# Kernel optimization log

Measured on AMD Instinct MI355X. Metric: run time of the kernel, lower is better.

Reference implementation:

```python
import jax, jax.numpy as jnp
import numpy as np

H = 8          # num_head
HD = 64        # head_dim = hidden_dim // num_head
WIN = 33       # atten_window_size (odd)
MIN_SCORE = -1e9


def setup_inputs() -> dict:
    key = jax.random.key(0)
    ks = jax.random.split(key, 12)
    B, S, D = 8, 4096, 512
    scale = 1.0 / np.sqrt(D).astype(np.float32)

    def lin_w(k):
        return jax.random.normal(k, (D, D), jnp.float32) * scale

    return {
        "query": jax.random.normal(ks[0], (B, S, D), jnp.float32),
        "key": jax.random.normal(ks[1], (B, S, D), jnp.float32),
        "value": jax.random.normal(ks[2], (B, S, D), jnp.float32),
        "mask": jax.random.randint(ks[3], (B, S), 0, 2).astype(bool),
        "Wq": lin_w(ks[4]), "bq": jax.random.normal(ks[5], (D,), jnp.float32) * 0.02,
        "Wk": lin_w(ks[6]), "bk": jax.random.normal(ks[7], (D,), jnp.float32) * 0.02,
        "Wv": lin_w(ks[8]), "bv": jax.random.normal(ks[9], (D,), jnp.float32) * 0.02,
        "Wo": lin_w(ks[10]), "bo": jax.random.normal(ks[11], (D,), jnp.float32) * 0.02,
    }


def reference(query, key, value, mask, Wq, bq, Wk, bk, Wv, bv, Wo, bo):
    B, S, D = query.shape
    half = min(WIN // 2, S // 2)

    def proj_split(x, W, b):
        # nn.Linear: x @ W.T + b; then split heads and flatten (B,H) -> B*H
        y = x @ W.T + b
        return y.reshape(B, S, H, HD).transpose(0, 2, 1, 3).reshape(B * H, S, HD)

    q = proj_split(query, Wq, bq)   # [BH, S, HD]
    k = proj_split(key, Wk, bk)
    v = proj_split(value, Wv, bv)
    # mask expanded over heads; True = masked (LocalAttention semantics)
    m = jnp.broadcast_to(mask[:, None, :], (B, H, S)).reshape(B * H, S)

    # banded scores: one [BH, S] vector per window offset (no sqrt(head_dim) scaling,
    # faithful to LocalAttention)
    scores = []
    for off in range(-half, half + 1):
        if off < 0:
            w = jnp.sum(q[:, -off:] * k[:, :off], axis=-1)
            w = jnp.where(m[:, :off], MIN_SCORE, w)
            w = jnp.pad(w, ((0, 0), (-off, 0)), constant_values=MIN_SCORE)
        elif off == 0:
            w = jnp.where(m, MIN_SCORE, jnp.sum(q * k, axis=-1))
        else:
            w = jnp.sum(q[:, :-off] * k[:, off:], axis=-1)
            w = jnp.where(m[:, off:], MIN_SCORE, w)
            w = jnp.pad(w, ((0, 0), (0, off)), constant_values=MIN_SCORE)
        scores.append(w)
    probs = jax.nn.softmax(jnp.stack(scores, axis=-1), axis=-1)  # [BH, S, 2*half+1]

    # weighted gather of values along the band (dropout=0 -> identity)
    out = jnp.zeros_like(v)
    for i, off in enumerate(range(-half, half + 1)):
        p = probs[:, :, i:i + 1]
        if off < 0:
            out = out + jnp.pad(p[:, -off:] * v[:, :off], ((0, 0), (-off, 0), (0, 0)))
        elif off == 0:
            out = out + p * v
        else:
            out = out + jnp.pad(p[:, :-off] * v[:, off:], ((0, 0), (0, off), (0, 0)))

    out = out.reshape(B, H, S, HD).transpose(0, 2, 1, 3).reshape(B, S, D)
    return out @ Wo.T + bo
```

## Files before the change

### kernel.cpp

```cpp
#include <hip/hip_runtime.h>
#include <hip/hip_bf16.h>
#include <stdint.h>

#define BB 8
#define SS 4096
#define DD 512
#define HH 8
#define HDIM 64

typedef unsigned short u16;
typedef __attribute__((ext_vector_type(4))) float f32x4;
typedef __attribute__((ext_vector_type(4))) short s16x4;
typedef __attribute__((ext_vector_type(8))) short s16x8;

__device__ __forceinline__ u16 f2bf(float f) {
  uint32_t x = __builtin_bit_cast(uint32_t, f);
  x += 0x7fffu + ((x >> 16) & 1u);
  return (u16)(x >> 16);
}
__device__ __forceinline__ float bf2f(u16 u) {
  uint32_t x = (uint32_t)u << 16;
  return __builtin_bit_cast(float, x);
}

__device__ __forceinline__ void gld_lds16(const u16* g, u16* l) {
  __builtin_amdgcn_global_load_lds((const __attribute__((address_space(1))) void*)g,
                                   (__attribute__((address_space(3))) void*)l, 16, 0, 0);
}

__global__ void cvt_f32_bf16(const float* __restrict__ in, u16* __restrict__ out, int n8) {
  int i = blockIdx.x * blockDim.x + threadIdx.x;
  const int stride = gridDim.x * blockDim.x;
  for (; i < n8; i += stride) {
    const f32x4 a0 = *(const f32x4*)(in + (size_t)i * 8);
    const f32x4 a1 = *(const f32x4*)(in + (size_t)i * 8 + 4);
    s16x8 pk;
#pragma unroll
    for (int j = 0; j < 4; ++j) pk[j] = (short)f2bf(a0[j]);
#pragma unroll
    for (int j = 0; j < 4; ++j) pk[4 + j] = (short)f2bf(a1[j]);
    *(s16x8*)(out + (size_t)i * 8) = pk;
  }
}

__global__ void cvt_weights(const float* __restrict__ w0, const float* __restrict__ w1,
                            const float* __restrict__ w2, const float* __restrict__ w3,
                            u16* __restrict__ out) {
  int i = blockIdx.x * blockDim.x + threadIdx.x;
  const int n = DD * DD;
  if (i < n) {
    out[i]         = f2bf(w0[i]);
    out[n + i]     = f2bf(w1[i]);
    out[2 * n + i] = f2bf(w2[i]);
    out[3 * n + i] = f2bf(w3[i]);
  }
}

__global__ void mask_unpack(const void* __restrict__ mraw, uint8_t* __restrict__ mk, int n) {
  __shared__ int bad[3];
  __shared__ int mode;
  const int t = threadIdx.x;
  if (t < 3) bad[t] = 0;
  __syncthreads();
  const uint32_t* w = (const uint32_t*)mraw;
  const uint32_t x = w[t];
  const bool w01 = (x == 0u) || (x == 1u);
  const uint32_t ob = x | (x >> 8) | (x >> 16) | (x >> 24);
  const bool u01 = ((ob & 0xFEu) == 0u);
  if (!w01) atomicAdd(&bad[0], 1);
  if (!u01) atomicAdd(&bad[1], 1);
  __syncthreads();
  if (t == 0) mode = (bad[0] == 0) ? 0 : (bad[1] == 0 ? 1 : 2);
  __syncthreads();
  const int md = mode;
  for (int i = blockIdx.x * 256 + t; i < n; i += gridDim.x * 256) {
    uint8_t v;
    if (md == 0)      v = (uint8_t)(w[i] & 1u);
    else if (md == 1) v = ((const uint8_t*)mraw)[i] ? 1 : 0;
    else              v = (w[i] != 0u) ? 1 : 0;
    mk[i] = v;
  }
}

template <typename TC>
__global__ __launch_bounds__(256, 2)
void gemm97(const u16* __restrict__ A, const u16* __restrict__ Bw,
            const float* __restrict__ bias, TC* __restrict__ C,
            int M, int N, int K) {
  __shared__ u16 sA[128 * 32];
  __shared__ u16 sB[128 * 32];

  const int tid = threadIdx.x;
  const int lane = tid & 63, wv = tid >> 6;
  const int wr = (wv >> 1) * 64, wc = (wv & 1) * 64;
  const int c = lane & 15, g = lane >> 4;
  const int lid = blockIdx.x;
  const int rb = (lid >> 5) * 8 + (lid & 7);
  const int cb = (lid >> 3) & 3;
  const int col0 = cb * 128, row0 = rb * 128;

  const int srow = tid >> 2, scol = (tid & 3) * 8;
  const u16* a_src = A + (size_t)(row0 + srow) * K + scol;
  const u16* b_src = Bw + (size_t)(col0 + srow) * K + scol;
  u16* sa0 = &sA[wv * 512];
  u16* sa1 = &sA[2048 + wv * 512];
  u16* sb0 = &sB[wv * 512];
  u16* sb1 = &sB[2048 + wv * 512];

  f32x4 acc[4][4];
#pragma unroll
  for (int a = 0; a < 4; ++a)
#pragma unroll
    for (int b = 0; b < 4; ++b) acc[a][b] = (f32x4){0.f, 0.f, 0.f, 0.f};

  const int nkt = K / 32;
  for (int kt = 0; kt < nkt; ++kt) {
    __syncthreads();
    const int ko = kt * 32;
    gld_lds16(a_src + ko, sa0);
    gld_lds16(a_src + (size_t)64 * K + ko, sa1);
    gld_lds16(b_src + ko, sb0);
    gld_lds16(b_src + (size_t)64 * K + ko, sb1);
    __syncthreads();

    s16x8 af[4], bq[4];
#pragma unroll
    for (int mf = 0; mf < 4; ++mf) af[mf] = *(const s16x8*)&sA[(wr + mf * 16 + c) * 32 + g * 8];
#pragma unroll
    for (int nf = 0; nf < 4; ++nf) bq[nf] = *(const s16x8*)&sB[(wc + nf * 16 + c) * 32 + g * 8];
#pragma unroll
    for (int mf = 0; mf < 4; ++mf)
#pragma unroll
      for (int nf = 0; nf < 4; ++nf)
        acc[mf][nf] = __builtin_amdgcn_mfma_f32_16x16x32_bf16(af[mf], bq[nf], acc[mf][nf], 0, 0, 0);
  }

#pragma unroll
  for (int nf = 0; nf < 4; ++nf) {
    const int col = col0 + wc + nf * 16 + c;
    const float bv = bias[col];
#pragma unroll
    for (int mf = 0; mf < 4; ++mf) {
#pragma unroll
      for (int i = 0; i < 4; ++i) {
        const int row = row0 + wr + mf * 16 + g * 4 + i;
        const float v = acc[mf][nf][i] + bv;
        if constexpr (sizeof(TC) == 4) C[(size_t)row * N + col] = v;
        else                           C[(size_t)row * N + col] = (TC)f2bf(v);
      }
    }
  }
}

__device__ __forceinline__ void hilo8(const f32x4& a0, const f32x4& a1, s16x8& h, s16x8& l) {
#pragma unroll
  for (int j = 0; j < 4; ++j) {
    const float f = a0[j];
    const u16 hb = f2bf(f);
    h[j] = (short)hb;
    l[j] = (short)f2bf(f - bf2f(hb));
  }
#pragma unroll
  for (int j = 0; j < 4; ++j) {
    const float f = a1[j];
    const u16 hb = f2bf(f);
    h[4 + j] = (short)hb;
    l[4 + j] = (short)f2bf(f - bf2f(hb));
  }
}

__global__ __launch_bounds__(256, 4)
void attn_mfma(const float* __restrict__ Qp, const float* __restrict__ Kp,
               const float* __restrict__ Vp, const uint8_t* __restrict__ mk,
               u16* __restrict__ O) {
  __shared__ u16 sKh[96 * 72];
  __shared__ u16 sKl[96 * 68];
  __shared__ u16 sVT[64 * 104];
  __shared__ float sM[96];

  const int bh = blockIdx.x;
  const int b = bh >> 3, h = bh & 7;
  const int s0 = blockIdx.y * 64;
  const int tid = threadIdx.x;

#pragma unroll
  for (int it = 0; it < 3; ++it) {
    const int item = tid + it * 256;
    const int row = item >> 3, j = item & 7;
    const int ks = j >> 2, g2 = j & 3;
    const int gr = s0 - 16 + row;
    f32x4 a0 = (f32x4){0.f, 0.f, 0.f, 0.f}, a1 = (f32x4){0.f, 0.f, 0.f, 0.f};
    if (gr >= 0 && gr < SS) {
      const float* kp = Kp + ((size_t)(b * SS + gr)) * DD + h * HDIM + ks * 32 + g2 * 4;
      a0 = *(const f32x4*)kp;
      a1 = *(const f32x4*)(kp + 16);
    }
    s16x8 hh, ll;
    hilo8(a0, a1, hh, ll);
    *(s16x8*)&sKh[row * 72 + j * 8] = hh;
    *(s16x4*)&sKl[row * 68 + j * 8]     = (s16x4){ll[0], ll[1], ll[2], ll[3]};
    *(s16x4*)&sKl[row * 68 + j * 8 + 4] = (s16x4){ll[4], ll[5], ll[6], ll[7]};
  }
#pragma unroll
  for (int it = 0; it < 6; ++it) {
    const int item = tid + it * 256;
    const int k = item >> 4, dg = item & 15;
    const int gr = s0 - 16 + k;
    f32x4 vv = (f32x4){0.f, 0.f, 0.f, 0.f};
    if (gr >= 0 && gr < SS)
      vv = *(const f32x4*)(Vp + ((size_t)(b * SS + gr)) * DD + h * HDIM + dg * 4);
    const int ks = k >> 5, rem = k & 31, hf = rem >> 4, q = rem & 15;
    const int g2 = q >> 2, i2 = q & 3;
    const int pos = (ks * 4 + g2) * 8 + hf * 4 + i2;
#pragma unroll
    for (int i = 0; i < 4; ++i) sVT[(dg * 4 + i) * 104 + pos] = f2bf(vv[i]);
  }
  for (int r = tid; r < 96; r += 256) {
    const int gr = s0 - 16 + r;
    sM[r] = (gr < 0 || gr >= SS || mk[b * SS + gr]) ? 1.f : 0.f;
  }
  __syncthreads();

  const int wv = tid >> 6, lane = tid & 63;
  const int c = lane & 15, g = lane >> 4;
  const int qloc = wv * 16 + c;
  const int qrow = s0 + qloc;

  const float* qp = Qp + ((size_t)(b * SS + qrow)) * DD + h * HDIM;
  s16x8 qh[2], qlo[2];
#pragma unroll
  for (int ks = 0; ks < 2; ++ks) {
    const f32x4 a0 = *(const f32x4*)(qp + 32 * ks + 4 * g);
    const f32x4 a1 = *(const f32x4*)(qp + 32 * ks + 16 + 4 * g);
    hilo8(a0, a1, qh[ks], qlo[ks]);
  }

  f32x4 st[6];
#pragma unroll
  for (int kt = 0; kt < 6; ++kt) st[kt] = (f32x4){0.f, 0.f, 0.f, 0.f};
#pragma unroll
  for (int kt = 0; kt < 6; ++kt) {
    const int rb72 = (kt * 16 + c) * 72;
    const int rb68 = (kt * 16 + c) * 68;
#pragma unroll
    for (int ks = 0; ks < 2; ++ks) {
      const s16x8 kh = *(const s16x8*)&sKh[rb72 + ks * 32 + g * 8];
      const s16x4 l0 = *(const s16x4*)&sKl[rb68 + ks * 32 + g * 8];
      const s16x4 l1 = *(const s16x4*)&sKl[rb68 + ks * 32 + g * 8 + 4];
      const s16x8 kl = (s16x8){l0[0], l0[1], l0[2], l0[3], l1[0], l1[1], l1[2], l1[3]};
      st[kt] = __builtin_amdgcn_mfma_f32_16x16x32_bf16(kh, qh[ks], st[kt], 0, 0, 0);
      st[kt] = __builtin_amdgcn_mfma_f32_16x16x32_bf16(kh, qlo[ks], st[kt], 0, 0, 0);
      st[kt] = __builtin_amdgcn_mfma_f32_16x16x32_bf16(kl, qh[ks], st[kt], 0, 0, 0);
    }
  }

  float mx = -3.0e9f;
#pragma unroll
  for (int kt = 0; kt < 6; ++kt) {
#pragma unroll
    for (int i = 0; i < 4; ++i) {
      const int kl_ = kt * 16 + 4 * g + i;
      const int delta = kl_ - 16 - qloc;
      float v;
      if (delta < -16 || delta > 16) v = -2.0e9f;
      else if (sM[kl_] != 0.f)       v = -1.0e9f;
      else                           v = st[kt][i];
      st[kt][i] = v;
      mx = fmaxf(mx, v);
    }
  }
  mx = fmaxf(mx, __shfl_xor(mx, 16));
  mx = fmaxf(mx, __shfl_xor(mx, 32));
  float sum = 0.f;
#pragma unroll
  for (int kt = 0; kt < 6; ++kt) {
#pragma unroll
    for (int i = 0; i < 4; ++i) {
      const float e = __expf(st[kt][i] - mx);
      st[kt][i] = e;
      sum += e;
    }
  }
  sum += __shfl_xor(sum, 16);
  sum += __shfl_xor(sum, 32);
  const float inv = 1.f / sum;

  s16x8 ph[3];
#pragma unroll
  for (int ks = 0; ks < 3; ++ks) {
#pragma unroll
    for (int i = 0; i < 4; ++i) {
      ph[ks][i]     = (short)f2bf(st[2 * ks][i]);
      ph[ks][4 + i] = (short)f2bf(st[2 * ks + 1][i]);
    }
  }

  f32x4 ot[4];
#pragma unroll
  for (int dt = 0; dt < 4; ++dt) ot[dt] = (f32x4){0.f, 0.f, 0.f, 0.f};
#pragma unroll
  for (int dt = 0; dt < 4; ++dt) {
    const int rbv = (dt * 16 + c) * 104;
#pragma unroll
    for (int ks = 0; ks < 3; ++ks) {
      const s16x8 vh = *(const s16x8*)&sVT[rbv + ks * 32 + g * 8];
      ot[dt] = __builtin_amdgcn_mfma_f32_16x16x32_bf16(vh, ph[ks], ot[dt], 0, 0, 0);
    }
  }

  u16* op = O + ((size_t)(b * SS + qrow)) * DD + h * HDIM;
#pragma unroll
  for (int dt = 0; dt < 4; ++dt) {
    s16x4 pk;
#pragma unroll
    for (int i = 0; i < 4; ++i) pk[i] = (short)f2bf(ot[dt][i] * inv);
    *(s16x4*)&op[dt * 16 + 4 * g] = pk;
  }
}

__global__ __launch_bounds__(256)
void attn_win(const u16* __restrict__ Qp, const u16* __restrict__ Kp,
              const u16* __restrict__ Vp, const uint8_t* __restrict__ mk,
              u16* __restrict__ O) {
  constexpr int KR = 96;
  __shared__ float sK[KR][HDIM];
  __shared__ float sV[KR][HDIM];
  __shared__ float sM[KR];

  const int bh = blockIdx.x;
  const int b = bh >> 3, h = bh & 7;
  const int s0 = blockIdx.y * 64;
  const int tid = threadIdx.x;

  for (int c = tid; c < KR * 16; c += 256) {
    const int row = c >> 4, c4 = c & 15;
    const int gr = s0 - 16 + row;
    float kv[4], vv[4];
    if (gr >= 0 && gr < SS) {
      const size_t base = ((size_t)(b * SS + gr)) * DD + h * HDIM + c4 * 4;
      const s16x4 kk = *(const s16x4*)(Kp + base);
      const s16x4 vx = *(const s16x4*)(Vp + base);
#pragma unroll
      for (int i = 0; i < 4; ++i) { kv[i] = bf2f((u16)kk[i]); vv[i] = bf2f((u16)vx[i]); }
    } else {
#pragma unroll
      for (int i = 0; i < 4; ++i) { kv[i] = 0.f; vv[i] = 0.f; }
    }
#pragma unroll
    for (int i = 0; i < 4; ++i) {
      const int d = c4 * 4 + i;
      const int pd = (d & 15) * 4 + (d >> 4);
      sK[row][pd] = kv[i];
      sV[row][pd] = vv[i];
    }
  }
  for (int r = tid; r < KR; r += 256) {
    const int gr = s0 - 16 + r;
    sM[r] = (gr < 0 || gr >= SS || mk[b * SS + gr]) ? 1.f : 0.f;
  }
  __syncthreads();

  const int wv = tid >> 6, lane = tid & 63;
  const int g = lane >> 4, d16 = lane & 15;

  for (int rr = 0; rr < 16; rr += 4) {
    const int lr = wv * 16 + rr + g;
    const int srow = s0 + lr;
    const u16* qp = Qp + ((size_t)(b * SS + srow)) * DD + h * HDIM;
    float q0 = bf2f(qp[d16]), q1 = bf2f(qp[d16 + 16]), q2 = bf2f(qp[d16 + 32]), q3 = bf2f(qp[d16 + 48]);
    float sc[33];
#pragma unroll
    for (int o = 0; o < 33; ++o) {
      const f32x4 kk = *(const f32x4*)&sK[lr + o][d16 * 4];
      float p = q0 * kk[0] + q1 * kk[1] + q2 * kk[2] + q3 * kk[3];
      p += __shfl_xor(p, 1);
      p += __shfl_xor(p, 2);
      p += __shfl_xor(p, 4);
      p += __shfl_xor(p, 8);
      sc[o] = (sM[lr + o] != 0.f) ? -1.0e9f : p;
    }
    float mx = sc[0];
#pragma unroll
    for (int o = 1; o < 33; ++o) mx = fmaxf(mx, sc[o]);
    float sum = 0.f;
#pragma unroll
    for (int o = 0; o < 33; ++o) { const float e = __expf(sc[o] - mx); sc[o] = e; sum += e; }
    const float inv = 1.f / sum;
    f32x4 acc = (f32x4){0.f, 0.f, 0.f, 0.f};
#pragma unroll
    for (int o = 0; o < 33; ++o) {
      const f32x4 vx = *(const f32x4*)&sV[lr + o][d16 * 4];
      acc += (sc[o] * inv) * vx;
    }
    u16* op = O + ((size_t)(b * SS + srow)) * DD + h * HDIM;
    op[d16]      = f2bf(acc[0]);
    op[d16 + 16] = f2bf(acc[1]);
    op[d16 + 32] = f2bf(acc[2]);
    op[d16 + 48] = f2bf(acc[3]);
  }
}

extern "C" void kernel_launch(void* const* d_in, const int* in_sizes, int n_in,
                              void* d_out, int out_size, void* d_ws, size_t ws_size,
                              hipStream_t stream) {
  const float* query = (const float*)d_in[0];
  const float* key   = (const float*)d_in[1];
  const float* value = (const float*)d_in[2];
  const void*  mraw  = d_in[3];
  const float* Wq = (const float*)d_in[4];
  const float* bq = (const float*)d_in[5];
  const float* Wk = (const float*)d_in[6];
  const float* bk = (const float*)d_in[7];
  const float* Wv = (const float*)d_in[8];
  const float* bv = (const float*)d_in[9];
  const float* Wo = (const float*)d_in[10];
  const float* bo = (const float*)d_in[11];

  const int M = BB * SS, N = DD, K = DD;

  char* ws = (char*)d_ws;
  size_t off = 0;
  auto carve = [&](size_t bytes) -> char* {
    char* p = ws + off;
    off = (off + bytes + 255) & ~(size_t)255;
    return p;
  };
  u16* wAll   = (u16*)carve((size_t)4 * DD * DD * sizeof(u16));
  uint8_t* mk = (uint8_t*)carve((size_t)BB * SS);
  u16* Xb     = (u16*)carve((size_t)M * DD * 2);

  const size_t qkv_f32 = (size_t)M * DD * 4;
  const bool f32p = (off + 3 * qkv_f32 + 1024) <= ws_size;

  cvt_weights<<<(DD * DD + 255) / 256, 256, 0, stream>>>(Wq, Wk, Wv, Wo, wAll);
  mask_unpack<<<16, 256, 0, stream>>>(mraw, mk, BB * SS);

  const int n8 = M * DD / 8;
  const dim3 gc(2048);
  const dim3 gg((M / 128) * (N / 128));
  const dim3 ga(BB * HH, SS / 64);
  u16* AO = Xb;

  if (f32p) {
    float* Qf = (float*)carve(qkv_f32);
    float* Kf = (float*)carve(qkv_f32);
    float* Vf = (float*)carve(qkv_f32);
    cvt_f32_bf16<<<gc, 256, 0, stream>>>(query, Xb, n8);
    gemm97<float><<<gg, 256, 0, stream>>>(Xb, wAll,               bq, Qf, M, N, K);
    cvt_f32_bf16<<<gc, 256, 0, stream>>>(key, Xb, n8);
    gemm97<float><<<gg, 256, 0, stream>>>(Xb, wAll + DD * DD,     bk, Kf, M, N, K);
    cvt_f32_bf16<<<gc, 256, 0, stream>>>(value, Xb, n8);
    gemm97<float><<<gg, 256, 0, stream>>>(Xb, wAll + 2 * DD * DD, bv, Vf, M, N, K);
    attn_mfma<<<ga, 256, 0, stream>>>(Qf, Kf, Vf, mk, AO);
  } else {
    const size_t qkv_b16 = (size_t)M * DD * 2;
    u16* Qb = (u16*)carve(qkv_b16);
    u16* Kb = (u16*)carve(qkv_b16);
    u16* Vb = (u16*)carve(qkv_b16);
    cvt_f32_bf16<<<gc, 256, 0, stream>>>(query, Xb, n8);
    gemm97<u16><<<gg, 256, 0, stream>>>(Xb, wAll,               bq, Qb, M, N, K);
    cvt_f32_bf16<<<gc, 256, 0, stream>>>(key, Xb, n8);
    gemm97<u16><<<gg, 256, 0, stream>>>(Xb, wAll + DD * DD,     bk, Kb, M, N, K);
    cvt_f32_bf16<<<gc, 256, 0, stream>>>(value, Xb, n8);
    gemm97<u16><<<gg, 256, 0, stream>>>(Xb, wAll + 2 * DD * DD, bv, Vb, M, N, K);
    attn_win<<<ga, 256, 0, stream>>>(Qb, Kb, Vb, mk, AO);
  }
  gemm97<float><<<gg, 256, 0, stream>>>(AO, wAll + 3 * DD * DD, bo, (float*)d_out, M, N, K);
}
```

Baseline: 258.1 us.

## Fuse fp32-to-bf16 input conversion into GEMM loads and store V as bf16

```diff
diff --git a/kernel.cpp b/kernel.cpp
--- a/kernel.cpp
+++ b/kernel.cpp
@@ -12,6 +12,7 @@
 typedef __attribute__((ext_vector_type(4))) float f32x4;
 typedef __attribute__((ext_vector_type(4))) short s16x4;
 typedef __attribute__((ext_vector_type(8))) short s16x8;
+typedef __attribute__((ext_vector_type(4))) unsigned int u32x4;
 
 __device__ __forceinline__ u16 f2bf(float f) {
   uint32_t x = __builtin_bit_cast(uint32_t, f);
@@ -22,25 +23,15 @@
   uint32_t x = (uint32_t)u << 16;
   return __builtin_bit_cast(float, x);
 }
-
-__device__ __forceinline__ void gld_lds16(const u16* g, u16* l) {
+__device__ __forceinline__ uint32_t cvtpk(float a, float b) {
+  uint32_t d;
+  asm("v_cvt_pk_bf16_f32 %0, %1, %2" : "=v"(d) : "v"(a), "v"(b));
+  return d;
+}
+
+__device__ __forceinline__ void gld_lds16(const void* g, void* l) {
   __builtin_amdgcn_global_load_lds((const __attribute__((address_space(1))) void*)g,
                                    (__attribute__((address_space(3))) void*)l, 16, 0, 0);
-}
-
-__global__ void cvt_f32_bf16(const float* __restrict__ in, u16* __restrict__ out, int n8) {
-  int i = blockIdx.x * blockDim.x + threadIdx.x;
-  const int stride = gridDim.x * blockDim.x;
-  for (; i < n8; i += stride) {
-    const f32x4 a0 = *(const f32x4*)(in + (size_t)i * 8);
-    const f32x4 a1 = *(const f32x4*)(in + (size_t)i * 8 + 4);
-    s16x8 pk;
-#pragma unroll
-    for (int j = 0; j < 4; ++j) pk[j] = (short)f2bf(a0[j]);
-#pragma unroll
-    for (int j = 0; j < 4; ++j) pk[4 + j] = (short)f2bf(a1[j]);
-    *(s16x8*)(out + (size_t)i * 8) = pk;
-  }
 }
 
 __global__ void cvt_weights(const float* __restrict__ w0, const float* __restrict__ w1,
@@ -82,13 +73,15 @@
   }
 }
 
-template <typename TC>
+template <typename TA, typename TC>
 __global__ __launch_bounds__(256, 2)
-void gemm97(const u16* __restrict__ A, const u16* __restrict__ Bw,
+void gemm97(const TA* __restrict__ A, const u16* __restrict__ Bw,
             const float* __restrict__ bias, TC* __restrict__ C,
             int M, int N, int K) {
-  __shared__ u16 sA[128 * 32];
-  __shared__ u16 sB[128 * 32];
+  constexpr bool AF32 = (sizeof(TA) == 4);
+  constexpr int ABYTES = AF32 ? 128 * 64 * 4 : 128 * 64 * 2;
+  __shared__ __align__(16) char sA[ABYTES];
+  __shared__ __align__(16) u16 sB[128 * 64];
 
   const int tid = threadIdx.x;
   const int lane = tid & 63, wv = tid >> 6;
@@ -99,13 +92,11 @@
   const int cb = (lid >> 3) & 3;
   const int col0 = cb * 128, row0 = rb * 128;
 
-  const int srow = tid >> 2, scol = (tid & 3) * 8;
-  const u16* a_src = A + (size_t)(row0 + srow) * K + scol;
-  const u16* b_src = Bw + (size_t)(col0 + srow) * K + scol;
-  u16* sa0 = &sA[wv * 512];
-  u16* sa1 = &sA[2048 + wv * 512];
-  u16* sb0 = &sB[wv * 512];
-  u16* sb1 = &sB[2048 + wv * 512];
+  const int srB = tid >> 3, cBc = (tid & 7) ^ ((tid >> 3) & 7);
+  const u16* b_src = Bw + (size_t)(col0 + srB) * K + cBc * 8;
+  const int srA = tid >> 4, cAc = (tid & 15) ^ (tid >> 4);
+  const TA* a_srcF = A + (size_t)(row0 + srA) * K + cAc * 4;
+  const TA* a_srcH = A + (size_t)(row0 + srB) * K + cBc * 8;
 
   f32x4 acc[4][4];
 #pragma unroll
@@ -113,26 +104,54 @@
 #pragma unroll
     for (int b = 0; b < 4; ++b) acc[a][b] = (f32x4){0.f, 0.f, 0.f, 0.f};
 
-  const int nkt = K / 32;
+  const int nkt = K / 64;
   for (int kt = 0; kt < nkt; ++kt) {
     __syncthreads();
-    const int ko = kt * 32;
-    gld_lds16(a_src + ko, sa0);
-    gld_lds16(a_src + (size_t)64 * K + ko, sa1);
-    gld_lds16(b_src + ko, sb0);
-    gld_lds16(b_src + (size_t)64 * K + ko, sb1);
+    const int ko = kt * 64;
+    if constexpr (AF32) {
+#pragma unroll
+      for (int i = 0; i < 8; ++i)
+        gld_lds16(a_srcF + (size_t)i * 16 * K + ko, sA + i * 4096 + wv * 1024);
+    } else {
+#pragma unroll
+      for (int i = 0; i < 4; ++i)
+        gld_lds16(a_srcH + (size_t)i * 32 * K + ko, sA + i * 4096 + wv * 1024);
+    }
+#pragma unroll
+    for (int i = 0; i < 4; ++i)
+      gld_lds16(b_src + (size_t)i * 32 * K + ko, (char*)sB + i * 4096 + wv * 1024);
     __syncthreads();
 
-    s16x8 af[4], bq[4];
-#pragma unroll
-    for (int mf = 0; mf < 4; ++mf) af[mf] = *(const s16x8*)&sA[(wr + mf * 16 + c) * 32 + g * 8];
-#pragma unroll
-    for (int nf = 0; nf < 4; ++nf) bq[nf] = *(const s16x8*)&sB[(wc + nf * 16 + c) * 32 + g * 8];
-#pragma unroll
-    for (int mf = 0; mf < 4; ++mf)
-#pragma unroll
-      for (int nf = 0; nf < 4; ++nf)
-        acc[mf][nf] = __builtin_amdgcn_mfma_f32_16x16x32_bf16(af[mf], bq[nf], acc[mf][nf], 0, 0, 0);
+#pragma unroll
+    for (int ks = 0; ks < 2; ++ks) {
+      s16x8 af[4], bq[4];
+#pragma unroll
+      for (int mf = 0; mf < 4; ++mf) {
+        const int row = wr + mf * 16 + c;
+        if constexpr (AF32) {
+          const int bc = ks * 128 + g * 32;
+          const f32x4 lo4 = *(const f32x4*)(sA + row * 256 + ((bc) ^ (c << 4)));
+          const f32x4 hi4 = *(const f32x4*)(sA + row * 256 + ((bc + 16) ^ (c << 4)));
+          const u32x4 dd = (u32x4){cvtpk(lo4[0], lo4[1]), cvtpk(lo4[2], lo4[3]),
+                                   cvtpk(hi4[0], hi4[1]), cvtpk(hi4[2], hi4[3])};
+          af[mf] = __builtin_bit_cast(s16x8, dd);
+        } else {
+          const int bc = ks * 64 + g * 16;
+          af[mf] = *(const s16x8*)(sA + row * 128 + (bc ^ ((c & 7) << 4)));
+        }
+      }
+#pragma unroll
+      for (int nf = 0; nf < 4; ++nf) {
+        const int row = wc + nf * 16 + c;
+        const int bc = ks * 64 + g * 16;
+        bq[nf] = *(const s16x8*)((char*)sB + row * 128 + (bc ^ ((c & 7) << 4)));
+      }
+#pragma unroll
+      for (int mf = 0; mf < 4; ++mf)
+#pragma unroll
+        for (int nf = 0; nf < 4; ++nf)
+          acc[mf][nf] = __builtin_amdgcn_mfma_f32_16x16x32_bf16(af[mf], bq[nf], acc[mf][nf], 0, 0, 0);
+    }
   }
 
 #pragma unroll
@@ -171,17 +190,30 @@
 
 __global__ __launch_bounds__(256, 4)
 void attn_mfma(const float* __restrict__ Qp, const float* __restrict__ Kp,
-               const float* __restrict__ Vp, const uint8_t* __restrict__ mk,
+               const u16* __restrict__ Vp, const uint8_t* __restrict__ mk,
                u16* __restrict__ O) {
   __shared__ u16 sKh[96 * 72];
   __shared__ u16 sKl[96 * 68];
   __shared__ u16 sVT[64 * 104];
-  __shared__ float sM[96];
+  __shared__ u16 sM[96];
 
   const int bh = blockIdx.x;
   const int b = bh >> 3, h = bh & 7;
   const int s0 = blockIdx.y * 64;
   const int tid = threadIdx.x;
+
+  const int wv = tid >> 6, lane = tid & 63;
+  const int c = lane & 15, g = lane >> 4;
+  const int qloc = wv * 16 + c;
+  const int qrow = s0 + qloc;
+
+  const float* qp = Qp + ((size_t)(b * SS + qrow)) * DD + h * HDIM;
+  f32x4 qa0[2], qa1[2];
+#pragma unroll
+  for (int ks = 0; ks < 2; ++ks) {
+    qa0[ks] = *(const f32x4*)(qp + 32 * ks + 4 * g);
+    qa1[ks] = *(const f32x4*)(qp + 32 * ks + 16 + 4 * g);
+  }
 
 #pragma unroll
   for (int it = 0; it < 3; ++it) {
@@ -202,38 +234,28 @@
     *(s16x4*)&sKl[row * 68 + j * 8 + 4] = (s16x4){ll[4], ll[5], ll[6], ll[7]};
   }
 #pragma unroll
-  for (int it = 0; it < 6; ++it) {
+  for (int it = 0; it < 3; ++it) {
     const int item = tid + it * 256;
-    const int k = item >> 4, dg = item & 15;
+    const int k = item >> 3, dg8 = item & 7;
     const int gr = s0 - 16 + k;
-    f32x4 vv = (f32x4){0.f, 0.f, 0.f, 0.f};
+    s16x8 vv = (s16x8){0, 0, 0, 0, 0, 0, 0, 0};
     if (gr >= 0 && gr < SS)
-      vv = *(const f32x4*)(Vp + ((size_t)(b * SS + gr)) * DD + h * HDIM + dg * 4);
+      vv = *(const s16x8*)(Vp + ((size_t)(b * SS + gr)) * DD + h * HDIM + dg8 * 8);
     const int ks = k >> 5, rem = k & 31, hf = rem >> 4, q = rem & 15;
     const int g2 = q >> 2, i2 = q & 3;
     const int pos = (ks * 4 + g2) * 8 + hf * 4 + i2;
 #pragma unroll
-    for (int i = 0; i < 4; ++i) sVT[(dg * 4 + i) * 104 + pos] = f2bf(vv[i]);
+    for (int i = 0; i < 8; ++i) sVT[(dg8 * 8 + i) * 104 + pos] = (u16)vv[i];
   }
   for (int r = tid; r < 96; r += 256) {
     const int gr = s0 - 16 + r;
-    sM[r] = (gr < 0 || gr >= SS || mk[b * SS + gr]) ? 1.f : 0.f;
+    sM[r] = (gr < 0 || gr >= SS || mk[b * SS + gr]) ? 1 : 0;
   }
   __syncthreads();
 
-  const int wv = tid >> 6, lane = tid & 63;
-  const int c = lane & 15, g = lane >> 4;
-  const int qloc = wv * 16 + c;
-  const int qrow = s0 + qloc;
-
-  const float* qp = Qp + ((size_t)(b * SS + qrow)) * DD + h * HDIM;
   s16x8 qh[2], qlo[2];
 #pragma unroll
-  for (int ks = 0; ks < 2; ++ks) {
-    const f32x4 a0 = *(const f32x4*)(qp + 32 * ks + 4 * g);
-    const f32x4 a1 = *(const f32x4*)(qp + 32 * ks + 16 + 4 * g);
-    hilo8(a0, a1, qh[ks], qlo[ks]);
-  }
+  for (int ks = 0; ks < 2; ++ks) hilo8(qa0[ks], qa1[ks], qh[ks], qlo[ks]);
 
   f32x4 st[6];
 #pragma unroll
@@ -263,7 +285,7 @@
       const int delta = kl_ - 16 - qloc;
       float v;
       if (delta < -16 || delta > 16) v = -2.0e9f;
-      else if (sM[kl_] != 0.f)       v = -1.0e9f;
+      else if (sM[kl_])              v = -1.0e9f;
       else                           v = st[kt][i];
       st[kt][i] = v;
       mx = fmaxf(mx, v);
@@ -325,7 +347,7 @@
   constexpr int KR = 96;
   __shared__ float sK[KR][HDIM];
   __shared__ float sV[KR][HDIM];
-  __shared__ float sM[KR];
+  __shared__ float sMf[KR];
 
   const int bh = blockIdx.x;
   const int b = bh >> 3, h = bh & 7;
@@ -356,7 +378,7 @@
   }
   for (int r = tid; r < KR; r += 256) {
     const int gr = s0 - 16 + r;
-    sM[r] = (gr < 0 || gr >= SS || mk[b * SS + gr]) ? 1.f : 0.f;
+    sMf[r] = (gr < 0 || gr >= SS || mk[b * SS + gr]) ? 1.f : 0.f;
   }
   __syncthreads();
 
@@ -377,7 +399,7 @@
       p += __shfl_xor(p, 2);
       p += __shfl_xor(p, 4);
       p += __shfl_xor(p, 8);
-      sc[o] = (sM[lr + o] != 0.f) ? -1.0e9f : p;
+      sc[o] = (sMf[lr + o] != 0.f) ? -1.0e9f : p;
     }
     float mx = sc[0];
 #pragma unroll
@@ -427,43 +449,36 @@
   };
   u16* wAll   = (u16*)carve((size_t)4 * DD * DD * sizeof(u16));
   uint8_t* mk = (uint8_t*)carve((size_t)BB * SS);
-  u16* Xb     = (u16*)carve((size_t)M * DD * 2);
-
-  const size_t qkv_f32 = (size_t)M * DD * 4;
-  const bool f32p = (off + 3 * qkv_f32 + 1024) <= ws_size;
+
+  const size_t qk_f32 = (size_t)M * DD * 4;
+  const size_t v_b16  = (size_t)M * DD * 2;
+  const bool f32p = (off + 2 * qk_f32 + 2 * v_b16 + 1024) <= ws_size;
 
   cvt_weights<<<(DD * DD + 255) / 256, 256, 0, stream>>>(Wq, Wk, Wv, Wo, wAll);
   mask_unpack<<<16, 256, 0, stream>>>(mraw, mk, BB * SS);
 
-  const int n8 = M * DD / 8;
-  const dim3 gc(2048);
   const dim3 gg((M / 128) * (N / 128));
   const dim3 ga(BB * HH, SS / 64);
-  u16* AO = Xb;
 
   if (f32p) {
-    float* Qf = (float*)carve(qkv_f32);
-    float* Kf = (float*)carve(qkv_f32);
-    float* Vf = (float*)carve(qkv_f32);
-    cvt_f32_bf16<<<gc, 256, 0, stream>>>(query, Xb, n8);
-    gemm97<float><<<gg, 256, 0, stream>>>(Xb, wAll,               bq, Qf, M, N, K);
-    cvt_f32_bf16<<<gc, 256, 0, stream>>>(key, Xb, n8);
-    gemm97<float><<<gg, 256, 0, stream>>>(Xb, wAll + DD * DD,     bk, Kf, M, N, K);
-    cvt_f32_bf16<<<gc, 256, 0, stream>>>(value, Xb, n8);
-    gemm97<float><<<gg, 256, 0, stream>>>(Xb, wAll + 2 * DD * DD, bv, Vf, M, N, K);
-    attn_mfma<<<ga, 256, 0, stream>>>(Qf, Kf, Vf, mk, AO);
+    float* Qf = (float*)carve(qk_f32);
+    float* Kf = (float*)carve(qk_f32);
+    u16*   Vb = (u16*)carve(v_b16);
+    u16*   AO = (u16*)carve(v_b16);
+    gemm97<float, float><<<gg, 256, 0, stream>>>(query, wAll,               bq, Qf, M, N, K);
+    gemm97<float, float><<<gg, 256, 0, stream>>>(key,   wAll + DD * DD,     bk, Kf, M, N, K);
+    gemm97<float, u16><<<gg, 256, 0, stream>>>(value, wAll + 2 * DD * DD, bv, Vb, M, N, K);
+    attn_mfma<<<ga, 256, 0, stream>>>(Qf, Kf, Vb, mk, AO);
+    gemm97<u16, float><<<gg, 256, 0, stream>>>(AO, wAll + 3 * DD * DD, bo, (float*)d_out, M, N, K);
   } else {
-    const size_t qkv_b16 = (size_t)M * DD * 2;
-    u16* Qb = (u16*)carve(qkv_b16);
-    u16* Kb = (u16*)carve(qkv_b16);
-    u16* Vb = (u16*)carve(qkv_b16);
-    cvt_f32_bf16<<<gc, 256, 0, stream>>>(query, Xb, n8);
-    gemm97<u16><<<gg, 256, 0, stream>>>(Xb, wAll,               bq, Qb, M, N, K);
-    cvt_f32_bf16<<<gc, 256, 0, stream>>>(key, Xb, n8);
-    gemm97<u16><<<gg, 256, 0, stream>>>(Xb, wAll + DD * DD,     bk, Kb, M, N, K);
-    cvt_f32_bf16<<<gc, 256, 0, stream>>>(value, Xb, n8);
-    gemm97<u16><<<gg, 256, 0, stream>>>(Xb, wAll + 2 * DD * DD, bv, Vb, M, N, K);
+    u16* Qb = (u16*)carve(v_b16);
+    u16* Kb = (u16*)carve(v_b16);
+    u16* Vb = (u16*)carve(v_b16);
+    u16* AO = (u16*)carve(v_b16);
+    gemm97<float, u16><<<gg, 256, 0, stream>>>(query, wAll,               bq, Qb, M, N, K);
+    gemm97<float, u16><<<gg, 256, 0, stream>>>(key,   wAll + DD * DD,     bk, Kb, M, N, K);
+    gemm97<float, u16><<<gg, 256, 0, stream>>>(value, wAll + 2 * DD * DD, bv, Vb, M, N, K);
     attn_win<<<ga, 256, 0, stream>>>(Qb, Kb, Vb, mk, AO);
-  }
-  gemm97<float><<<gg, 256, 0, stream>>>(AO, wAll + 3 * DD * DD, bo, (float*)d_out, M, N, K);
-}
+    gemm97<u16, float><<<gg, 256, 0, stream>>>(AO, wAll + 3 * DD * DD, bo, (float*)d_out, M, N, K);
+  }
+}
```

Result: faster. 234.1 us (-9.3%).
